# Optimization experiments

Hardware: AMD Instinct MI355X
Metric: run time of the kernel (lower is better)

## Reference

```python
import jax, jax.numpy as jnp
import numpy as np

D = 1024
B, S = 4, 2048

def setup_inputs() -> dict:
    key = jax.random.key(0)
    ks = jax.random.split(key, 4)
    scale = 1.0 / np.sqrt(D)
    return {
        "x": jax.random.normal(ks[0], (B, S, D), dtype=jnp.float32),
        "Wq": jax.random.normal(ks[1], (D, D), dtype=jnp.float32) * scale,
        "bq": jnp.zeros((D,), jnp.float32),
        "Wk": jax.random.normal(ks[2], (D, D), dtype=jnp.float32) * scale,
        "bk": jnp.zeros((D,), jnp.float32),
        "Wv": jax.random.normal(ks[3], (D, D), dtype=jnp.float32) * scale,
        "bv": jnp.zeros((D,), jnp.float32),
    }

def reference(x, Wq, bq, Wk, bk, Wv, bv):
    # torch Linear: y = x @ W.T + b
    Q = jnp.einsum('bsd,ed->bse', x, Wq) + bq
    K = jnp.einsum('bsd,ed->bse', x, Wk) + bk
    V = jnp.einsum('bsd,ed->bse', x, Wv) + bv
    # NOTE: original scales by sqrt(K.shape[1]) == sqrt(seq_len), kept faithfully
    dk = K.shape[1]
    logits = jnp.einsum('bqd,bkd->bqk', Q, K) / jnp.sqrt(jnp.asarray(dk, Q.dtype))
    att = jax.nn.softmax(logits, axis=-1)
    return jnp.einsum('bqk,bkd->bqd', att, V)
```

## Files before the change

### kernel.cpp

```cpp
#include <hip/hip_runtime.h>


typedef unsigned short u16;
typedef unsigned int u32;
typedef __bf16 bf16x8 __attribute__((ext_vector_type(8)));
typedef float floatx4 __attribute__((ext_vector_type(4)));

__device__ __forceinline__ u16 f2bf(float f) {
    u32 u = __float_as_uint(f);
    u += 0x7fffu + ((u >> 16) & 1u);
    return (u16)(u >> 16);
}

__device__ __forceinline__ void g2lds16(const void* g, void* l) {
    __builtin_amdgcn_global_load_lds(
        (const __attribute__((address_space(1))) unsigned int*)g,
        (__attribute__((address_space(3))) unsigned int*)l,
        16, 0, 0);
}

__global__ __launch_bounds__(256)
void cvt_f32_bf16(const float* __restrict__ in, u16* __restrict__ out, int n4) {
    int i = blockIdx.x * 256 + threadIdx.x;
    if (i >= n4) return;
    float4 v = ((const float4*)in)[i];
    ushort4 o;
    o.x = f2bf(v.x); o.y = f2bf(v.y); o.z = f2bf(v.z); o.w = f2bf(v.w);
    ((ushort4*)out)[i] = o;
}

template<int MODE>
__global__ __launch_bounds__(256)
void gemm_bt(const u16* __restrict__ A, const u16* __restrict__ B,
             void* __restrict__ Out, const float* __restrict__ bias,
             float scale, int M, int N, int K,
             long long sAz, long long sBz, long long sOz)
{
    __shared__ u16 ldsA[128 * 64];
    __shared__ u16 ldsB[128 * 64];

    const int tid   = threadIdx.x;
    const int lane  = tid & 63;
    const int wv    = tid >> 6;
    const int wm    = (wv >> 1) * 64;
    const int wn    = (wv & 1) * 64;
    const int lhalf = lane & 15;
    const int quad  = lane >> 4;

    const size_t bz = blockIdx.z;
    A += bz * (size_t)sAz;
    B += bz * (size_t)sBz;

    int tm, tn;
    {
        const int ntn = gridDim.x, ntm = gridDim.y;
        const int lin = blockIdx.y * ntn + blockIdx.x;
        const int GM = 4;
        const int width = GM * ntn;
        const int group = lin / width;
        const int first = group * GM;
        const int gsz   = (ntm - first) < GM ? (ntm - first) : GM;
        const int rem   = lin - group * width;
        tm = first + rem % gsz;
        tn = rem / gsz;
    }
    const int m0 = tm * 128;
    const int n0 = tn * 128;

    const int r8 = lane >> 3;
    const int gc = (lane & 7) ^ r8;
    const u16* pa = A + (size_t)(m0 + wv * 32 + r8) * K + gc * 8;
    const u16* pb = B + (size_t)(n0 + wv * 32 + r8) * K + gc * 8;
    u16* la = ldsA + wv * 2048;
    u16* lb = ldsB + wv * 2048;

    floatx4 zero = {0.f, 0.f, 0.f, 0.f};
    floatx4 acc[4][4];
#pragma unroll
    for (int i = 0; i < 4; ++i)
#pragma unroll
        for (int j = 0; j < 4; ++j) acc[i][j] = zero;

    const int swz = lhalf & 7;

    for (int k0 = 0; k0 < K; k0 += 64) {
        __syncthreads();
#pragma unroll
        for (int j = 0; j < 4; ++j) {
            g2lds16(pa + (size_t)(j * 8) * K, la + j * 512);
            g2lds16(pb + (size_t)(j * 8) * K, lb + j * 512);
        }
        pa += 64; pb += 64;
        __syncthreads();

#pragma unroll
        for (int ks = 0; ks < 2; ++ks) {
            bf16x8 af[4], bf[4];
            const int c = ks * 4 + quad;
            const int p = c ^ swz;
#pragma unroll
            for (int i = 0; i < 4; ++i)
                af[i] = *(const bf16x8*)(ldsA + (wm + i * 16 + lhalf) * 64 + p * 8);
#pragma unroll
            for (int j = 0; j < 4; ++j)
                bf[j] = *(const bf16x8*)(ldsB + (wn + j * 16 + lhalf) * 64 + p * 8);
#pragma unroll
            for (int i = 0; i < 4; ++i)
#pragma unroll
                for (int j = 0; j < 4; ++j)
                    acc[i][j] = __builtin_amdgcn_mfma_f32_16x16x32_bf16(
                        af[i], bf[j], acc[i][j], 0, 0, 0);
        }
    }

#pragma unroll
    for (int i = 0; i < 4; ++i) {
        const int mb = m0 + wm + i * 16 + quad * 4;
#pragma unroll
        for (int j = 0; j < 4; ++j) {
            const int n = n0 + wn + j * 16 + lhalf;
            const float bb = bias ? bias[n] : 0.f;
#pragma unroll
            for (int r = 0; r < 4; ++r) {
                const int m = mb + r;
                const float v = acc[i][j][r] * scale + bb;
                if (MODE == 2) {
                    ((float*)Out)[bz * (size_t)sOz + (size_t)m * N + n] = v;
                } else if (MODE == 0) {
                    ((u16*)Out)[bz * (size_t)sOz + (size_t)m * N + n] = f2bf(v);
                } else {
                    ((u16*)Out)[bz * (size_t)sOz + (size_t)n * M + m] = f2bf(v);
                }
            }
        }
    }
}

__global__ __launch_bounds__(256)
void softmax_rows(u16* __restrict__ S)
{
    const int tid = threadIdx.x;
    u16* row = S + (size_t)blockIdx.x * 2048;
    uint4 v = ((const uint4*)row)[tid];
    float x[8];
    x[0] = __uint_as_float(v.x << 16); x[1] = __uint_as_float(v.x & 0xffff0000u);
    x[2] = __uint_as_float(v.y << 16); x[3] = __uint_as_float(v.y & 0xffff0000u);
    x[4] = __uint_as_float(v.z << 16); x[5] = __uint_as_float(v.z & 0xffff0000u);
    x[6] = __uint_as_float(v.w << 16); x[7] = __uint_as_float(v.w & 0xffff0000u);

    float mx = x[0];
#pragma unroll
    for (int i = 1; i < 8; ++i) mx = fmaxf(mx, x[i]);
#pragma unroll
    for (int off = 32; off > 0; off >>= 1) mx = fmaxf(mx, __shfl_xor(mx, off, 64));

    __shared__ float sm[4], ss[4];
    if ((tid & 63) == 0) sm[tid >> 6] = mx;
    __syncthreads();
    mx = fmaxf(fmaxf(sm[0], sm[1]), fmaxf(sm[2], sm[3]));

    float e[8];
    float s = 0.f;
#pragma unroll
    for (int i = 0; i < 8; ++i) { e[i] = __expf(x[i] - mx); s += e[i]; }
#pragma unroll
    for (int off = 32; off > 0; off >>= 1) s += __shfl_xor(s, off, 64);
    if ((tid & 63) == 0) ss[tid >> 6] = s;
    __syncthreads();
    s = (ss[0] + ss[1]) + (ss[2] + ss[3]);

    const float inv = 1.f / s;
    uint4 o;
    o.x = (u32)f2bf(e[0] * inv) | ((u32)f2bf(e[1] * inv) << 16);
    o.y = (u32)f2bf(e[2] * inv) | ((u32)f2bf(e[3] * inv) << 16);
    o.z = (u32)f2bf(e[4] * inv) | ((u32)f2bf(e[5] * inv) << 16);
    o.w = (u32)f2bf(e[6] * inv) | ((u32)f2bf(e[7] * inv) << 16);
    ((uint4*)row)[tid] = o;
}

extern "C" void kernel_launch(void* const* d_in, const int* in_sizes, int n_in,
                              void* d_out, int out_size, void* d_ws, size_t ws_size,
                              hipStream_t stream)
{
    const float* x  = (const float*)d_in[0];
    const float* Wq = (const float*)d_in[1];
    const float* bq = (const float*)d_in[2];
    const float* Wk = (const float*)d_in[3];
    const float* bk = (const float*)d_in[4];
    const float* Wv = (const float*)d_in[5];
    const float* bv = (const float*)d_in[6];
    float* out = (float*)d_out;

    const int B = 4, S = 2048, D = 1024;
    const long long SD = (long long)S * D;
    const long long SS = (long long)S * S;
    const long long BSD = (long long)B * SD;
    const long long DD = (long long)D * D;

    u16* xb  = (u16*)d_ws;
    u16* wqb = xb  + BSD;
    u16* wkb = wqb + DD;
    u16* wvb = wkb + DD;
    u16* Qb  = wvb + DD;
    u16* Kb  = Qb  + BSD;
    u16* Vt  = Kb  + BSD;
    u16* Sc  = Vt  + BSD;

    cvt_f32_bf16<<<dim3((int)(BSD / 4 / 256)), 256, 0, stream>>>(x,  xb,  (int)(BSD / 4));
    cvt_f32_bf16<<<dim3((int)(DD  / 4 / 256)), 256, 0, stream>>>(Wq, wqb, (int)(DD / 4));
    cvt_f32_bf16<<<dim3((int)(DD  / 4 / 256)), 256, 0, stream>>>(Wk, wkb, (int)(DD / 4));
    cvt_f32_bf16<<<dim3((int)(DD  / 4 / 256)), 256, 0, stream>>>(Wv, wvb, (int)(DD / 4));

    gemm_bt<0><<<dim3(D / 128, (B * S) / 128, 1), 256, 0, stream>>>(
        xb, wqb, Qb, bq, 1.f, B * S, D, D, 0, 0, 0);
    gemm_bt<0><<<dim3(D / 128, (B * S) / 128, 1), 256, 0, stream>>>(
        xb, wkb, Kb, bk, 1.f, B * S, D, D, 0, 0, 0);
    gemm_bt<1><<<dim3(D / 128, S / 128, B), 256, 0, stream>>>(
        xb, wvb, Vt, bv, 1.f, S, D, D, SD, 0, SD);

    const float sc = 0.022097086912079608f;
    gemm_bt<0><<<dim3(S / 128, S / 128, B), 256, 0, stream>>>(
        Qb, Kb, Sc, nullptr, sc, S, S, D, SD, SD, SS);

    softmax_rows<<<dim3(B * S), 256, 0, stream>>>(Sc);

    gemm_bt<2><<<dim3(D / 128, S / 128, B), 256, 0, stream>>>(
        Sc, Vt, out, nullptr, 1.f, S, D, S, SS, SD, SD);
}
```

Baseline: 289.2 us.

## Double-buffer LDS tiles in GEMM to overlap global loads with MFMA

Splits the LDS A/B tiles into two buffers and issues the async global-to-LDS loads for the next K tile before computing on the current one. This drops one barrier per iteration and aims to hide global load latency behind the MFMA work. LDS use per block doubles to 64 KB, which may lower occupancy. If the compiler conservatively waits on all outstanding vector-memory operations before the LDS reads, the loads would not actually overlap with compute.

Measured after the change: 271.8 us. 1.06x faster.

```diff
diff --git a/kernel.cpp b/kernel.cpp
--- a/kernel.cpp
+++ b/kernel.cpp
@@ -36,8 +36,8 @@
              float scale, int M, int N, int K,
              long long sAz, long long sBz, long long sOz)
 {
-    __shared__ u16 ldsA[128 * 64];
-    __shared__ u16 ldsB[128 * 64];
+    __shared__ u16 ldsA[2][128 * 64];
+    __shared__ u16 ldsB[2][128 * 64];
 
     const int tid   = threadIdx.x;
     const int lane  = tid & 63;
@@ -71,8 +71,7 @@
     const int gc = (lane & 7) ^ r8;
     const u16* pa = A + (size_t)(m0 + wv * 32 + r8) * K + gc * 8;
     const u16* pb = B + (size_t)(n0 + wv * 32 + r8) * K + gc * 8;
-    u16* la = ldsA + wv * 2048;
-    u16* lb = ldsB + wv * 2048;
+    const int lofs = wv * 2048;
 
     floatx4 zero = {0.f, 0.f, 0.f, 0.f};
     floatx4 acc[4][4];
@@ -83,34 +82,46 @@
 
     const int swz = lhalf & 7;
 
+#pragma unroll
+    for (int j = 0; j < 4; ++j) {
+        g2lds16(pa + (size_t)(j * 8) * K, &ldsA[0][lofs + j * 512]);
+        g2lds16(pb + (size_t)(j * 8) * K, &ldsB[0][lofs + j * 512]);
+    }
+    pa += 64; pb += 64;
+
+    int buf = 0;
     for (int k0 = 0; k0 < K; k0 += 64) {
         __syncthreads();
-#pragma unroll
-        for (int j = 0; j < 4; ++j) {
-            g2lds16(pa + (size_t)(j * 8) * K, la + j * 512);
-            g2lds16(pb + (size_t)(j * 8) * K, lb + j * 512);
+        if (k0 + 64 < K) {
+#pragma unroll
+            for (int j = 0; j < 4; ++j) {
+                g2lds16(pa + (size_t)(j * 8) * K, &ldsA[buf ^ 1][lofs + j * 512]);
+                g2lds16(pb + (size_t)(j * 8) * K, &ldsB[buf ^ 1][lofs + j * 512]);
+            }
+            pa += 64; pb += 64;
         }
-        pa += 64; pb += 64;
-        __syncthreads();
-
+
+        const u16* lA = ldsA[buf];
+        const u16* lB = ldsB[buf];
 #pragma unroll
         for (int ks = 0; ks < 2; ++ks) {
-            bf16x8 af[4], bf[4];
+            bf16x8 af[4], bfv[4];
             const int c = ks * 4 + quad;
             const int p = c ^ swz;
 #pragma unroll
             for (int i = 0; i < 4; ++i)
-                af[i] = *(const bf16x8*)(ldsA + (wm + i * 16 + lhalf) * 64 + p * 8);
+                af[i] = *(const bf16x8*)(lA + (wm + i * 16 + lhalf) * 64 + p * 8);
 #pragma unroll
             for (int j = 0; j < 4; ++j)
-                bf[j] = *(const bf16x8*)(ldsB + (wn + j * 16 + lhalf) * 64 + p * 8);
+                bfv[j] = *(const bf16x8*)(lB + (wn + j * 16 + lhalf) * 64 + p * 8);
 #pragma unroll
             for (int i = 0; i < 4; ++i)
 #pragma unroll
                 for (int j = 0; j < 4; ++j)
                     acc[i][j] = __builtin_amdgcn_mfma_f32_16x16x32_bf16(
-                        af[i], bf[j], acc[i][j], 0, 0, 0);
+                        af[i], bfv[j], acc[i][j], 0, 0, 0);
         }
+        buf ^= 1;
     }
 
 #pragma unroll
```
